# Optimization experiments

Measured on AMD Instinct MI355X. Metric: run time of the kernel, lower is better.

## Reference

```python
import jax, jax.numpy as jnp
import numpy as np

HIDDEN, LATENT, SYM, BOX = 512, 256, 64, 128
LEAF = 16384
NODE = 2 * LEAF - 1  # 32767: complete binary tree, leaves first
W_SCALE = 0.05  # keep tanh unsaturated


def setup_inputs() -> dict:
    key = jax.random.key(0)
    ks = jax.random.split(key, 16)
    # kids: valid tree structure (randint per-spec would give invalid child pointers).
    # Leaves are nodes [0, LEAF); internal node LEAF+j merges nodes 2j and 2j+1
    # (1-indexed pointers 2j+1, 2j+2). Every 4th internal node is a symmetry node.
    j = np.arange(NODE - LEAF)
    kids = np.zeros((1, NODE, 3), dtype=np.int32)
    kids[0, LEAF:, 0] = 2 * j + 1
    kids[0, LEAF:, 1] = 2 * j + 2
    kids[0, LEAF:, 2] = (j % 4 == 3).astype(np.int32)
    f32 = jnp.float32
    return {
        "kids": jnp.asarray(kids),
        "shape": jax.random.normal(ks[0], (1, BOX, LEAF), dtype=f32),
        "param": jax.random.normal(ks[1], (1, NODE, SYM), dtype=f32),
        # leaf / box encoder: box -> latent
        "Wb": jax.random.normal(ks[2], (BOX, LATENT), dtype=f32) * W_SCALE,
        "bb": jnp.zeros((LATENT,), dtype=f32),
        # adjacency encoder: (latent, latent) -> hidden -> latent
        "Wl": jax.random.normal(ks[3], (LATENT, HIDDEN), dtype=f32) * W_SCALE,
        "Wr": jax.random.normal(ks[4], (LATENT, HIDDEN), dtype=f32) * W_SCALE,
        "b1": jnp.zeros((HIDDEN,), dtype=f32),
        "W2": jax.random.normal(ks[5], (HIDDEN, LATENT), dtype=f32) * W_SCALE,
        "b2": jnp.zeros((LATENT,), dtype=f32),
        # symmetry encoder: (latent, sym) -> hidden -> latent
        "Wsl": jax.random.normal(ks[6], (LATENT, HIDDEN), dtype=f32) * W_SCALE,
        "Wsr": jax.random.normal(ks[7], (SYM, HIDDEN), dtype=f32) * W_SCALE,
        "bs1": jnp.zeros((HIDDEN,), dtype=f32),
        "Ws2": jax.random.normal(ks[8], (HIDDEN, LATENT), dtype=f32) * W_SCALE,
        "bs2": jnp.zeros((LATENT,), dtype=f32),
    }


def reference(kids, shape, param, Wb, bb, Wl, Wr, b1, W2, b2, Wsl, Wsr, bs1, Ws2, bs2):
    nodeNum = kids.shape[1]
    leafNum = shape.shape[2]
    latent = Wb.shape[1]

    # Leaves (nodes 0..leafNum-1, kids[...,0]==0) have no data dependence on hOut:
    # encode them all at once. boxes: [leafNum, box]
    boxes = jnp.transpose(shape[0])
    hLeaf = jnp.tanh(boxes @ Wb + bb)  # [leafNum, latent]
    hOut = jnp.zeros((nodeNum, latent), dtype=shape.dtype).at[:leafNum].set(hLeaf)

    p = param[0]  # [nodeNum, sym]
    k = kids[0]   # [nodeNum, 3]

    def step(h, x):
        i, k0, k1, k2 = x
        a = h[k0 - 1]      # [latent] left child hidden
        b = h[k1 - 1]      # [latent] right child hidden (adjacency case)
        s = p[k0 - 1]      # [sym]    (source indexes param with kids[...,0]-1)
        # adjacency merge
        h1 = jnp.tanh(jnp.tanh(a @ Wl + b @ Wr + b1) @ W2 + b2)
        # symmetry merge
        h2 = jnp.tanh(jnp.tanh(a @ Wsl + s @ Wsr + bs1) @ Ws2 + bs2)
        hi = jnp.where(k2 == 1, h2, h1)
        return h.at[i].set(hi), None

    # internal nodes are i in [leafNum, nodeNum); original only defines inputs there
    idx = jnp.arange(leafNum, nodeNum)
    xs = (idx, k[leafNum:, 0], k[leafNum:, 1], k[leafNum:, 2])
    hOut, _ = jax.lax.scan(step, hOut, xs)
    return hOut[nodeNum - 1][None, :]  # [1, latent], the root code
```

## Files before the change

kernel.cpp:

```cpp
#include <hip/hip_runtime.h>

#define LEAF   16384
#define NNODE  (2*LEAF-1)
#define LATENT 256
#define HIDDEN 512
#define SYM    64
#define BOX    128

using half8 = __attribute__((ext_vector_type(8))) _Float16;
using f32x4 = __attribute__((ext_vector_type(4))) float;

__device__ __forceinline__ f32x4 mfma16h(half8 a, half8 b, f32x4 c){
    return __builtin_amdgcn_mfma_f32_16x16x32_f16(a, b, c, 0, 0, 0);
}

__global__ void pack_kernel(const float* __restrict__ A, const float* __restrict__ B,
                            int Ksplit, int N, int KS, _Float16* __restrict__ pk, int total)
{
    int t = blockIdx.x*256 + threadIdx.x;
    if (t >= total) return;
    int j = t & 7, l = (t>>3)&63, tile = (t>>9)&3;
    int rest = t >> 11;
    int ks = rest % KS, cb = rest / KS;
    int k   = ks*32 + ((l>>4)*8) + j;
    int col = cb*64 + tile*16 + (l&15);
    float wv = (k < Ksplit) ? A[(size_t)k*N + col] : B[(size_t)(k-Ksplit)*N + col];
    pk[((size_t)(cb*KS + ks)*4 + tile)*512 + (size_t)l*8 + j] = (_Float16)wv;
}

__global__ __launch_bounds__(256) void leaf_mfma_kernel(
    const float* __restrict__ shape, const _Float16* __restrict__ wbpk,
    const float* __restrict__ bb, _Float16* __restrict__ hh)
{
    const int t = threadIdx.x, lane = t & 63, w = t >> 6;
    const int r0 = blockIdx.x * 64;
    const int m = r0 + w*16 + (lane & 15);

    half8 A[4];
    #pragma unroll
    for (int ks = 0; ks < 4; ++ks) {
        #pragma unroll
        for (int e = 0; e < 8; ++e) {
            int k = ks*32 + (lane >> 4)*8 + e;
            A[ks][e] = (_Float16)shape[(size_t)k*LEAF + m];
        }
    }

    for (int cb = 0; cb < 4; ++cb) {
        f32x4 acc[4];
        #pragma unroll
        for (int c = 0; c < 4; ++c) acc[c] = (f32x4){0.f,0.f,0.f,0.f};
        #pragma unroll
        for (int ks = 0; ks < 4; ++ks) {
            const _Float16* pb = wbpk + (size_t)((cb*4 + ks)*4)*512;
            #pragma unroll
            for (int tile = 0; tile < 4; ++tile) {
                half8 B = *(const half8*)(pb + tile*512 + lane*8);
                acc[tile] = mfma16h(A[ks], B, acc[tile]);
            }
        }
        #pragma unroll
        for (int tile = 0; tile < 4; ++tile) {
            int col = cb*64 + tile*16 + (lane & 15);
            float bv = bb[col];
            #pragma unroll
            for (int r = 0; r < 4; ++r) {
                int row = r0 + w*16 + (lane >> 4)*4 + r;
                hh[(size_t)row*256 + col] = (_Float16)tanhf(acc[tile][r] + bv);
            }
        }
    }
}

template<int NSUB>
__device__ __forceinline__ void k1_body(
    int rb, int cb, int start, int n,
    const _Float16* __restrict__ hh, const float* __restrict__ param,
    const _Float16* __restrict__ wcatpk, const _Float16* __restrict__ wscatpk,
    const float* __restrict__ b1, const float* __restrict__ bs1,
    _Float16* __restrict__ U, _Float16* __restrict__ V)
{
    __shared__ __align__(16) _Float16 ldsB1[2*2048];
    const int t = threadIdx.x, lane = t & 63, w = t >> 6;
    const bool isV = cb >= 8;
    const int cbl = isV ? cb - 8 : cb;
    const int KS  = isV ? 10 : 16;
    const _Float16* pk = (isV ? wscatpk : wcatpk) + (size_t)cbl * KS * 2048;
    const int row0  = rb * NSUB * 64;
    const int cbase = 2 * (start - LEAF);

    f32x4 acc[NSUB][4];
    #pragma unroll
    for (int s = 0; s < NSUB; ++s)
        #pragma unroll
        for (int c = 0; c < 4; ++c) acc[s][c] = (f32x4){0.f,0.f,0.f,0.f};

    *(half8*)(ldsB1 + t*8) = *(const half8*)(pk + (size_t)t*8);
    __syncthreads();

    for (int ks = 0; ks < KS; ++ks) {
        const bool hasNext = ks + 1 < KS;
        half8 stg;
        if (hasNext) stg = *(const half8*)(pk + (size_t)(ks+1)*2048 + (size_t)t*8);
        half8 A[NSUB];
        #pragma unroll
        for (int s = 0; s < NSUB; ++s) {
            int m = row0 + (s*4 + w)*16 + (lane & 15);
            if (m >= n) m = n - 1;
            if (!isV || ks < 8) {
                int node = cbase + 2*m + (ks >= 8 ? 1 : 0);
                A[s] = *(const half8*)(hh + (size_t)node*256 + (size_t)(ks & 7)*32 + ((lane >> 4)*8));
            } else {
                const float* pp = param + (size_t)(cbase + 2*m)*64 + (ks - 8)*32 + (lane >> 4)*8;
                float4 p0 = *(const float4*)pp;
                float4 p1 = *(const float4*)(pp + 4);
                A[s][0]=(_Float16)p0.x; A[s][1]=(_Float16)p0.y; A[s][2]=(_Float16)p0.z; A[s][3]=(_Float16)p0.w;
                A[s][4]=(_Float16)p1.x; A[s][5]=(_Float16)p1.y; A[s][6]=(_Float16)p1.z; A[s][7]=(_Float16)p1.w;
            }
        }
        const _Float16* lb = ldsB1 + (ks & 1)*2048;
        #pragma unroll
        for (int tile = 0; tile < 4; ++tile) {
            half8 Bh = *(const half8*)(lb + tile*512 + lane*8);
            #pragma unroll
            for (int s = 0; s < NSUB; ++s)
                acc[s][tile] = mfma16h(A[s], Bh, acc[s][tile]);
        }
        if (hasNext)
            *(half8*)(ldsB1 + ((ks+1) & 1)*2048 + t*8) = stg;
        __syncthreads();
    }

    const float* bias = isV ? bs1 : b1;
    _Float16* o = isV ? V : U;
    #pragma unroll
    for (int s = 0; s < NSUB; ++s) {
        #pragma unroll
        for (int tile = 0; tile < 4; ++tile) {
            int col = cbl*64 + tile*16 + (lane & 15);
            float bv = bias[col];
            #pragma unroll
            for (int r = 0; r < 4; ++r) {
                int m = row0 + (s*4 + w)*16 + (lane >> 4)*4 + r;
                if (m < n)
                    o[(size_t)m*512 + col] = (_Float16)tanhf(acc[s][tile][r] + bv);
            }
        }
    }
}

template<int NSUB>
__device__ __forceinline__ void k2_body(
    int rb, int cb, int start, int n,
    const _Float16* __restrict__ U, const _Float16* __restrict__ V,
    const int* __restrict__ kids,
    const _Float16* __restrict__ w2pk, const _Float16* __restrict__ ws2pk,
    const float* __restrict__ b2, const float* __restrict__ bs2,
    _Float16* __restrict__ hh)
{
    __shared__ __align__(16) _Float16 ldsB2[2*2048];
    const int t = threadIdx.x, lane = t & 63, w = t >> 6;
    const bool isSym = cb >= 4;
    const int cbl = isSym ? cb - 4 : cb;
    const _Float16* pk = (isSym ? ws2pk : w2pk) + (size_t)cbl * 16 * 2048;
    const _Float16* Asrc = isSym ? V : U;
    const int row0 = rb * NSUB * 64;

    f32x4 acc[NSUB][4];
    #pragma unroll
    for (int s = 0; s < NSUB; ++s)
        #pragma unroll
        for (int c = 0; c < 4; ++c) acc[s][c] = (f32x4){0.f,0.f,0.f,0.f};

    *(half8*)(ldsB2 + t*8) = *(const half8*)(pk + (size_t)t*8);
    __syncthreads();

    for (int ks = 0; ks < 16; ++ks) {
        const bool hasNext = ks + 1 < 16;
        half8 stg;
        if (hasNext) stg = *(const half8*)(pk + (size_t)(ks+1)*2048 + (size_t)t*8);
        half8 A[NSUB];
        #pragma unroll
        for (int s = 0; s < NSUB; ++s) {
            int m = row0 + (s*4 + w)*16 + (lane & 15);
            if (m >= n) m = n - 1;
            A[s] = *(const half8*)(Asrc + (size_t)m*512 + (size_t)ks*32 + ((lane >> 4)*8));
        }
        const _Float16* lb = ldsB2 + (ks & 1)*2048;
        #pragma unroll
        for (int tile = 0; tile < 4; ++tile) {
            half8 Bh = *(const half8*)(lb + tile*512 + lane*8);
            #pragma unroll
            for (int s = 0; s < NSUB; ++s)
                acc[s][tile] = mfma16h(A[s], Bh, acc[s][tile]);
        }
        if (hasNext)
            *(half8*)(ldsB2 + ((ks+1) & 1)*2048 + t*8) = stg;
        __syncthreads();
    }

    const float* bias = isSym ? bs2 : b2;
    const int want = isSym ? 1 : 0;
    #pragma unroll
    for (int s = 0; s < NSUB; ++s) {
        #pragma unroll
        for (int tile = 0; tile < 4; ++tile) {
            int col = cbl*64 + tile*16 + (lane & 15);
            float bv = bias[col];
            #pragma unroll
            for (int r = 0; r < 4; ++r) {
                int m = row0 + (s*4 + w)*16 + (lane >> 4)*4 + r;
                if (m < n && kids[3*(start + m) + 2] == want)
                    hh[(size_t)(start + m)*256 + col] = (_Float16)tanhf(acc[s][tile][r] + bv);
            }
        }
    }
}

template<int NSUB>
__global__ __launch_bounds__(256) void k1_kernel(
    const _Float16* __restrict__ hh, const float* __restrict__ param,
    const _Float16* __restrict__ wcatpk, const _Float16* __restrict__ wscatpk,
    const float* __restrict__ b1, const float* __restrict__ bs1,
    _Float16* __restrict__ U, _Float16* __restrict__ V, int start, int n)
{
    k1_body<NSUB>(blockIdx.x, blockIdx.y, start, n, hh, param, wcatpk, wscatpk, b1, bs1, U, V);
}

template<int NSUB>
__global__ __launch_bounds__(256) void k2_kernel(
    const _Float16* __restrict__ U, const _Float16* __restrict__ V,
    const int* __restrict__ kids,
    const _Float16* __restrict__ w2pk, const _Float16* __restrict__ ws2pk,
    const float* __restrict__ b2, const float* __restrict__ bs2,
    _Float16* __restrict__ hh, int start, int n)
{
    k2_body<NSUB>(blockIdx.x, blockIdx.y, start, n, U, V, kids, w2pk, ws2pk, b2, bs2, hh);
}

__device__ __forceinline__ void k1_tail(
    int rb, int cb, int start, int n,
    const _Float16* __restrict__ hh, const float* __restrict__ param,
    const _Float16* wlds,
    const float* __restrict__ b1, const float* __restrict__ bs1,
    _Float16* __restrict__ U, _Float16* __restrict__ V)
{
    const int t = threadIdx.x, lane = t & 63, w = t >> 6;
    const bool isV = cb >= 8;
    const int cbl = isV ? cb - 8 : cb;
    const int KS  = isV ? 10 : 16;
    const int row0  = rb * 64;
    const int cbase = 2 * (start - LEAF);

    f32x4 acc[4];
    #pragma unroll
    for (int c = 0; c < 4; ++c) acc[c] = (f32x4){0.f,0.f,0.f,0.f};

    int m = row0 + w*16 + (lane & 15);
    if (m >= n) m = n - 1;

    for (int ks = 0; ks < KS; ++ks) {
        half8 A;
        if (!isV || ks < 8) {
            int node = cbase + 2*m + (ks >= 8 ? 1 : 0);
            A = *(const half8*)(hh + (size_t)node*256 + (size_t)(ks & 7)*32 + ((lane >> 4)*8));
        } else {
            const float* pp = param + (size_t)(cbase + 2*m)*64 + (ks - 8)*32 + (lane >> 4)*8;
            float4 p0 = *(const float4*)pp;
            float4 p1 = *(const float4*)(pp + 4);
            A[0]=(_Float16)p0.x; A[1]=(_Float16)p0.y; A[2]=(_Float16)p0.z; A[3]=(_Float16)p0.w;
            A[4]=(_Float16)p1.x; A[5]=(_Float16)p1.y; A[6]=(_Float16)p1.z; A[7]=(_Float16)p1.w;
        }
        const _Float16* lb = wlds + ks*2048;
        #pragma unroll
        for (int tile = 0; tile < 4; ++tile) {
            half8 Bh = *(const half8*)(lb + tile*512 + lane*8);
            acc[tile] = mfma16h(A, Bh, acc[tile]);
        }
    }

    const float* bias = isV ? bs1 : b1;
    _Float16* o = isV ? V : U;
    #pragma unroll
    for (int tile = 0; tile < 4; ++tile) {
        int col = cbl*64 + tile*16 + (lane & 15);
        float bv = bias[col];
        #pragma unroll
        for (int r = 0; r < 4; ++r) {
            int mm = row0 + w*16 + (lane >> 4)*4 + r;
            if (mm < n)
                o[(size_t)mm*512 + col] = (_Float16)tanhf(acc[tile][r] + bv);
        }
    }
}

__device__ __forceinline__ void k2_tail(
    int rb, int cb, int start, int n,
    const _Float16* __restrict__ U, const _Float16* __restrict__ V,
    const int* __restrict__ kids,
    const _Float16* wlds,
    const float* __restrict__ b2, const float* __restrict__ bs2,
    _Float16* __restrict__ hh)
{
    const int t = threadIdx.x, lane = t & 63, w = t >> 6;
    const bool isSym = cb >= 4;
    const int cbl = isSym ? cb - 4 : cb;
    const _Float16* Asrc = isSym ? V : U;
    const int row0 = rb * 64;

    f32x4 acc[4];
    #pragma unroll
    for (int c = 0; c < 4; ++c) acc[c] = (f32x4){0.f,0.f,0.f,0.f};

    int m = row0 + w*16 + (lane & 15);
    if (m >= n) m = n - 1;

    for (int ks = 0; ks < 16; ++ks) {
        half8 A = *(const half8*)(Asrc + (size_t)m*512 + (size_t)ks*32 + ((lane >> 4)*8));
        const _Float16* lb = wlds + ks*2048;
        #pragma unroll
        for (int tile = 0; tile < 4; ++tile) {
            half8 Bh = *(const half8*)(lb + tile*512 + lane*8);
            acc[tile] = mfma16h(A, Bh, acc[tile]);
        }
    }

    const float* bias = isSym ? bs2 : b2;
    const int want = isSym ? 1 : 0;
    #pragma unroll
    for (int tile = 0; tile < 4; ++tile) {
        int col = cbl*64 + tile*16 + (lane & 15);
        float bv = bias[col];
        #pragma unroll
        for (int r = 0; r < 4; ++r) {
            int mm = row0 + w*16 + (lane >> 4)*4 + r;
            if (mm < n && kids[3*(start + mm) + 2] == want)
                hh[(size_t)(start + mm)*256 + col] = (_Float16)tanhf(acc[tile][r] + bv);
        }
    }
}

__device__ __forceinline__ void gbar(unsigned* bar, unsigned target)
{
    __syncthreads();
    if (threadIdx.x == 0) {
        __hip_atomic_fetch_add(bar, 1u, __ATOMIC_RELEASE, __HIP_MEMORY_SCOPE_AGENT);
        while (__hip_atomic_load(bar, __ATOMIC_RELAXED, __HIP_MEMORY_SCOPE_AGENT) < target)
            __builtin_amdgcn_s_sleep(4);
    }
    __syncthreads();
    __builtin_amdgcn_fence(__ATOMIC_ACQUIRE, "agent");
}

__global__ __launch_bounds__(256) void tail_kernel(
    _Float16* __restrict__ hh, const float* __restrict__ param,
    const _Float16* __restrict__ wcatpk, const _Float16* __restrict__ wscatpk,
    const float* __restrict__ b1, const float* __restrict__ bs1,
    _Float16* __restrict__ U, _Float16* __restrict__ V,
    const int* __restrict__ kids,
    const _Float16* __restrict__ w2pk, const _Float16* __restrict__ ws2pk,
    const float* __restrict__ b2, const float* __restrict__ bs2,
    unsigned* __restrict__ bar, float* __restrict__ out)
{
    __shared__ __align__(16) _Float16 wlds[16*2048];
    const int b = blockIdx.x;
    const int t = threadIdx.x;
    const bool isK1 = b < 32;
    int cb, rh;
    const _Float16* src;
    int nh;
    if (isK1) {
        cb = b & 15; rh = b >> 4;
        if (cb < 8) { src = wcatpk  + (size_t)cb*16*2048;     nh = 16*256; }
        else        { src = wscatpk + (size_t)(cb-8)*10*2048; nh = 10*256; }
    } else {
        int i = b - 32; cb = i & 7; rh = i >> 3;
        if (cb < 4) src = w2pk  + (size_t)cb*16*2048;
        else        src = ws2pk + (size_t)(cb-4)*16*2048;
        nh = 16*256;
    }
    for (int i = t; i < nh; i += 256)
        *(half8*)(wlds + (size_t)i*8) = *(const half8*)(src + (size_t)i*8);
    __syncthreads();

    const unsigned G = gridDim.x;
    unsigned tgt = 0;
    int start = LEAF + 8192 + 4096 + 2048 + 1024 + 512;
    for (int n = 256; n >= 1; n >>= 1) {
        int rt = (n + 63) >> 6;
        if (isK1) {
            for (int r = rh; r < rt; r += 2)
                k1_tail(r, cb, start, n, hh, param, wlds, b1, bs1, U, V);
        }
        tgt += G; gbar(bar, tgt);
        if (!isK1) {
            for (int r = rh; r < rt; r += 2)
                k2_tail(r, cb, start, n, U, V, kids, wlds, b2, bs2, hh);
        }
        tgt += G; gbar(bar, tgt);
        start += n;
    }
    if (b == 0)
        out[t] = (float)hh[(size_t)(NNODE - 1)*256 + t];
}

extern "C" void kernel_launch(void* const* d_in, const int* in_sizes, int n_in,
                              void* d_out, int out_size, void* d_ws, size_t ws_size,
                              hipStream_t stream) {
    const int*   kids  = (const int*)  d_in[0];
    const float* shape = (const float*)d_in[1];
    const float* param = (const float*)d_in[2];
    const float* Wb    = (const float*)d_in[3];
    const float* bb    = (const float*)d_in[4];
    const float* Wl    = (const float*)d_in[5];
    const float* Wr    = (const float*)d_in[6];
    const float* b1    = (const float*)d_in[7];
    const float* W2    = (const float*)d_in[8];
    const float* b2    = (const float*)d_in[9];
    const float* Wsl   = (const float*)d_in[10];
    const float* Wsr   = (const float*)d_in[11];
    const float* bs1   = (const float*)d_in[12];
    const float* Ws2   = (const float*)d_in[13];
    const float* bs2   = (const float*)d_in[14];
    float* out = (float*)d_out;

    char* ws = (char*)d_ws;
    _Float16* hh      = (_Float16*)(ws + 0);
    _Float16* U       = (_Float16*)(ws + 16777216);
    _Float16* V       = (_Float16*)(ws + 25165824);
    _Float16* wcatpk  = (_Float16*)(ws + 33554432);
    _Float16* wscatpk = (_Float16*)(ws + 34078720);
    _Float16* w2pk    = (_Float16*)(ws + 34406400);
    _Float16* ws2pk   = (_Float16*)(ws + 34668544);
    _Float16* wbpk    = (_Float16*)(ws + 34930688);
    unsigned* bar     = (unsigned*)(ws + 34996224);

    hipMemsetAsync(bar, 0, 256, stream);

    pack_kernel<<<1024, 256, 0, stream>>>(Wl,  Wr,  256, 512, 16, wcatpk,  262144);
    pack_kernel<<< 640, 256, 0, stream>>>(Wsl, Wsr, 256, 512, 10, wscatpk, 163840);
    pack_kernel<<< 512, 256, 0, stream>>>(W2,  W2,  512, 256, 16, w2pk,    131072);
    pack_kernel<<< 512, 256, 0, stream>>>(Ws2, Ws2, 512, 256, 16, ws2pk,   131072);
    pack_kernel<<< 128, 256, 0, stream>>>(Wb,  Wb,  128, 256,  4, wbpk,     32768);

    leaf_mfma_kernel<<<LEAF/64, 256, 0, stream>>>(shape, wbpk, bb, hh);

    int start = LEAF;
    for (int n = 8192; n >= 512; n >>= 1) {
        if (n == 8192) {
            k1_kernel<2><<<dim3(n/128, 16), 256, 0, stream>>>(hh, param, wcatpk, wscatpk,
                                                              b1, bs1, U, V, start, n);
        } else {
            k1_kernel<1><<<dim3(n/64, 16), 256, 0, stream>>>(hh, param, wcatpk, wscatpk,
                                                             b1, bs1, U, V, start, n);
        }
        k2_kernel<1><<<dim3(n/64, 8), 256, 0, stream>>>(U, V, kids, w2pk, ws2pk,
                                                        b2, bs2, hh, start, n);
        start += n;
    }

    tail_kernel<<<48, 256, 0, stream>>>(hh, param, wcatpk, wscatpk, b1, bs1,
                                        U, V, kids, w2pk, ws2pk, b2, bs2, bar, out);
}
```

Measured before the change: 361.0 us.

## Merge pack kernels, widen persistent tail, use per-block flag barrier

Fuses the five weight-pack launches into a single kernel and replaces the single-counter atomic grid barrier with per-block flag stores that every block polls. The persistent tail kernel grows from 48 to 96 blocks and now also handles the 1024 and 512 levels, so four fewer separate k1/k2 launches are issued. The goal is to cut launch overhead and barrier contention on the serial small levels. In exchange, the tail runs more barrier rounds, each thread polls 96 flags, and the persistent grid is larger.

```diff
diff --git a/kernel.cpp b/kernel.cpp
--- a/kernel.cpp
+++ b/kernel.cpp
@@ -14,11 +14,22 @@
     return __builtin_amdgcn_mfma_f32_16x16x32_f16(a, b, c, 0, 0, 0);
 }
 
-__global__ void pack_kernel(const float* __restrict__ A, const float* __restrict__ B,
-                            int Ksplit, int N, int KS, _Float16* __restrict__ pk, int total)
-{
-    int t = blockIdx.x*256 + threadIdx.x;
-    if (t >= total) return;
+__global__ void pack_all(const float* __restrict__ Wl, const float* __restrict__ Wr,
+                         const float* __restrict__ Wsl, const float* __restrict__ Wsr,
+                         const float* __restrict__ W2, const float* __restrict__ Ws2,
+                         const float* __restrict__ Wb,
+                         _Float16* __restrict__ wcat, _Float16* __restrict__ wscat,
+                         _Float16* __restrict__ w2p, _Float16* __restrict__ ws2p,
+                         _Float16* __restrict__ wbp)
+{
+    int g = blockIdx.x*256 + threadIdx.x;
+    const float *A, *B; _Float16* pk; int Ksplit, N, KS, t;
+    if (g < 262144)      { t = g;          A=Wl;  B=Wr;  pk=wcat;  Ksplit=256; N=512; KS=16; }
+    else if (g < 425984) { t = g-262144;   A=Wsl; B=Wsr; pk=wscat; Ksplit=256; N=512; KS=10; }
+    else if (g < 557056) { t = g-425984;   A=W2;  B=W2;  pk=w2p;   Ksplit=512; N=256; KS=16; }
+    else if (g < 688128) { t = g-557056;   A=Ws2; B=Ws2; pk=ws2p;  Ksplit=512; N=256; KS=16; }
+    else if (g < 720896) { t = g-688128;   A=Wb;  B=Wb;  pk=wbp;   Ksplit=128; N=256; KS=4;  }
+    else return;
     int j = t & 7, l = (t>>3)&63, tile = (t>>9)&3;
     int rest = t >> 11;
     int ks = rest % KS, cb = rest / KS;
@@ -340,13 +351,15 @@
     }
 }
 
-__device__ __forceinline__ void gbar(unsigned* bar, unsigned target)
+#define TAILG 96
+__device__ __forceinline__ void fbar(unsigned* flags, unsigned tgt)
 {
     __syncthreads();
-    if (threadIdx.x == 0) {
-        __hip_atomic_fetch_add(bar, 1u, __ATOMIC_RELEASE, __HIP_MEMORY_SCOPE_AGENT);
-        while (__hip_atomic_load(bar, __ATOMIC_RELAXED, __HIP_MEMORY_SCOPE_AGENT) < target)
-            __builtin_amdgcn_s_sleep(4);
+    if (threadIdx.x == 0)
+        __hip_atomic_store(flags + blockIdx.x*16, tgt, __ATOMIC_RELEASE, __HIP_MEMORY_SCOPE_AGENT);
+    if (threadIdx.x < TAILG) {
+        while (__hip_atomic_load(flags + threadIdx.x*16, __ATOMIC_RELAXED, __HIP_MEMORY_SCOPE_AGENT) < tgt)
+            __builtin_amdgcn_s_sleep(1);
     }
     __syncthreads();
     __builtin_amdgcn_fence(__ATOMIC_ACQUIRE, "agent");
@@ -360,12 +373,12 @@
     const int* __restrict__ kids,
     const _Float16* __restrict__ w2pk, const _Float16* __restrict__ ws2pk,
     const float* __restrict__ b2, const float* __restrict__ bs2,
-    unsigned* __restrict__ bar, float* __restrict__ out)
+    unsigned* __restrict__ flags, float* __restrict__ out)
 {
     __shared__ __align__(16) _Float16 wlds[16*2048];
     const int b = blockIdx.x;
     const int t = threadIdx.x;
-    const bool isK1 = b < 32;
+    const bool isK1 = b < 64;
     int cb, rh;
     const _Float16* src;
     int nh;
@@ -374,7 +387,7 @@
         if (cb < 8) { src = wcatpk  + (size_t)cb*16*2048;     nh = 16*256; }
         else        { src = wscatpk + (size_t)(cb-8)*10*2048; nh = 10*256; }
     } else {
-        int i = b - 32; cb = i & 7; rh = i >> 3;
+        int i = b - 64; cb = i & 7; rh = i >> 3;
         if (cb < 4) src = w2pk  + (size_t)cb*16*2048;
         else        src = ws2pk + (size_t)(cb-4)*16*2048;
         nh = 16*256;
@@ -383,21 +396,20 @@
         *(half8*)(wlds + (size_t)i*8) = *(const half8*)(src + (size_t)i*8);
     __syncthreads();
 
-    const unsigned G = gridDim.x;
     unsigned tgt = 0;
-    int start = LEAF + 8192 + 4096 + 2048 + 1024 + 512;
-    for (int n = 256; n >= 1; n >>= 1) {
+    int start = LEAF + 8192 + 4096 + 2048;
+    for (int n = 1024; n >= 1; n >>= 1) {
         int rt = (n + 63) >> 6;
         if (isK1) {
-            for (int r = rh; r < rt; r += 2)
+            for (int r = rh; r < rt; r += 4)
                 k1_tail(r, cb, start, n, hh, param, wlds, b1, bs1, U, V);
         }
-        tgt += G; gbar(bar, tgt);
+        ++tgt; fbar(flags, tgt);
         if (!isK1) {
-            for (int r = rh; r < rt; r += 2)
+            for (int r = rh; r < rt; r += 4)
                 k2_tail(r, cb, start, n, U, V, kids, wlds, b2, bs2, hh);
         }
-        tgt += G; gbar(bar, tgt);
+        ++tgt; fbar(flags, tgt);
         start += n;
     }
     if (b == 0)
@@ -433,20 +445,17 @@
     _Float16* w2pk    = (_Float16*)(ws + 34406400);
     _Float16* ws2pk   = (_Float16*)(ws + 34668544);
     _Float16* wbpk    = (_Float16*)(ws + 34930688);
-    unsigned* bar     = (unsigned*)(ws + 34996224);
-
-    hipMemsetAsync(bar, 0, 256, stream);
-
-    pack_kernel<<<1024, 256, 0, stream>>>(Wl,  Wr,  256, 512, 16, wcatpk,  262144);
-    pack_kernel<<< 640, 256, 0, stream>>>(Wsl, Wsr, 256, 512, 10, wscatpk, 163840);
-    pack_kernel<<< 512, 256, 0, stream>>>(W2,  W2,  512, 256, 16, w2pk,    131072);
-    pack_kernel<<< 512, 256, 0, stream>>>(Ws2, Ws2, 512, 256, 16, ws2pk,   131072);
-    pack_kernel<<< 128, 256, 0, stream>>>(Wb,  Wb,  128, 256,  4, wbpk,     32768);
+    unsigned* flags   = (unsigned*)(ws + 34996224);
+
+    hipMemsetAsync(flags, 0, TAILG*64, stream);
+
+    pack_all<<<2816, 256, 0, stream>>>(Wl, Wr, Wsl, Wsr, W2, Ws2, Wb,
+                                       wcatpk, wscatpk, w2pk, ws2pk, wbpk);
 
     leaf_mfma_kernel<<<LEAF/64, 256, 0, stream>>>(shape, wbpk, bb, hh);
 
     int start = LEAF;
-    for (int n = 8192; n >= 512; n >>= 1) {
+    for (int n = 8192; n >= 2048; n >>= 1) {
         if (n == 8192) {
             k1_kernel<2><<<dim3(n/128, 16), 256, 0, stream>>>(hh, param, wcatpk, wscatpk,
                                                               b1, bs1, U, V, start, n);
@@ -459,6 +468,6 @@
         start += n;
     }
 
-    tail_kernel<<<48, 256, 0, stream>>>(hh, param, wcatpk, wscatpk, b1, bs1,
-                                        U, V, kids, w2pk, ws2pk, b2, bs2, bar, out);
-}
+    tail_kernel<<<TAILG, 256, 0, stream>>>(hh, param, wcatpk, wscatpk, b1, bs1,
+                                           U, V, kids, w2pk, ws2pk, b2, bs2, flags, out);
+}
```

Result: slower. 416.4 us (+15.3%).
